# Kernel optimization log

Hardware: AMD Instinct MI355X
Metric: run time of the kernel (lower is better)

Reference implementation:

```python
import jax, jax.numpy as jnp
import numpy as np

B, T, C, NH = 4, 827, 1024, 16
HS = C // NH
SCALE = 1.0 / float(np.sqrt(HS))


def setup_inputs() -> dict:
    key = jax.random.key(0)
    ks = jax.random.split(key, 16)
    d = {}
    d["x"] = jax.random.normal(ks[0], (B, T, C), jnp.float32)
    d["x_kv"] = jax.random.normal(ks[1], (B, T, C), jnp.float32)
    d["h"] = jax.random.normal(ks[2], (B, NH, T, T), jnp.float32) * 0.1
    for i, name in enumerate(["f01", "f02", "f12", "b01", "b02", "b12"]):
        d[name] = jax.random.uniform(ks[3 + i], (B, 256, 256), jnp.float32)
    for i, name in enumerate(["Wq", "Wk", "Wv", "Wp"]):
        d[name] = jax.random.normal(ks[9 + i], (C, C), jnp.float32) * 0.02
    for name in ["bq", "bk", "bv", "bp"]:
        d[name] = jnp.zeros((C,), jnp.float32)
    return d


def _sm(a):
    return jax.nn.softmax(a, axis=-1)


def reference(x, x_kv, h, f01, f02, f12, b01, b02, b12,
              Wq, bq, Wk, bk, Wv, bv, Wp, bp):
    Bb, Tt, Cc = x.shape

    def heads(t):  # [B,T,C] -> [B,NH,T,HS]
        return t.reshape(Bb, Tt, NH, HS).transpose(0, 2, 1, 3)

    q = heads(x @ Wq.T + bq)
    k = heads(x_kv @ Wk.T + bk)
    v = heads(x_kv @ Wv.T + bv)

    att = jnp.einsum('bhqd,bhkd->bhqk', q, k) * SCALE + h  # adaptive bias add

    # region-specific partial softmax (frame1->frame0, frame2->frame0, frame2->frame1)
    att = att.at[:, :, 285:541, 0:256].set(_sm(att[:, :, 285:541, 0:256]))
    att = att.at[:, :, 571:827, 0:256].set(_sm(att[:, :, 571:827, 0:256]))
    att = att.at[:, :, 571:827, 286:542].set(_sm(att[:, :, 571:827, 286:542]))

    # bidirectional epipolar maps (backward maps used transposed)
    b01t = b01.transpose(0, 2, 1)
    b02t = b02.transpose(0, 2, 1)
    b12t = b12.transpose(0, 2, 1)
    m12 = (f12 * b12t >= 0.1).astype(att.dtype)  # [B,256,256]

    # bi_epi_ratio (T==827 branch), computed BEFORE the multiplicative masking
    r3 = att[:, :, 571:827, 286:542]            # [B,NH,256,256]
    att_mean = r3.mean(-1)                       # [B,NH,256]
    att_mask_mean = (r3 * m12[:, None]).sum(-1) / m12.sum(-1)[:, None]
    bi_epi_ratio = att_mask_mean.mean(1) / att_mean.mean(1)  # [B,256]

    # att_for: forward-only masking (clone); att: forward*backward masking
    att_for = att
    att_for = att_for.at[:, :, 285:541, 0:256].multiply(f01[:, None])
    att_for = att_for.at[:, :, 571:827, 0:256].multiply(f02[:, None])
    att_for = att_for.at[:, :, 571:827, 286:542].multiply(f12[:, None])
    att = att.at[:, :, 285:541, 0:256].multiply((b01t * f01)[:, None])
    att = att.at[:, :, 571:827, 0:256].multiply((b02t * f02)[:, None])
    att = att.at[:, :, 571:827, 286:542].multiply((b12t * f12)[:, None])

    causal = jnp.tril(jnp.ones((Tt, Tt), dtype=bool))
    aw = jnp.where(causal, att, -jnp.inf)
    # re-softmax of the already masked+multiplied regions (overwrites, then global softmax)
    aw = aw.at[:, :, 571:827, 0:256].set(_sm(att[:, :, 571:827, 0:256]))
    aw = aw.at[:, :, 571:827, 286:542].set(_sm(att[:, :, 571:827, 286:542]))
    aw = _sm(aw)

    y = jnp.einsum('bhqk,bhkd->bhqd', aw, v)
    y = y.transpose(0, 2, 1, 3).reshape(Bb, Tt, Cc)
    y = y @ Wp.T + bp  # resid dropout is identity (pdrop=0 / eval)
    return y, bi_epi_ratio
```

## Files before the change

### kernel.cpp

```cpp
#include <hip/hip_runtime.h>
#include <cstdint>
#include <cstddef>

#define Tn  827
#define Cn  1024
#define BTn 3308
#define TPn 832
#define YSZ 3387392

typedef unsigned short u16;
typedef unsigned short u16x4 __attribute__((ext_vector_type(4)));
typedef __bf16 bf16_t;
typedef bf16_t bf16x8 __attribute__((ext_vector_type(8)));
typedef float f32x4 __attribute__((ext_vector_type(4)));

#define GLD(gp, lp) __builtin_amdgcn_global_load_lds( \
    (__attribute__((address_space(1))) void*)(gp),    \
    (__attribute__((address_space(3))) void*)(lp), 16, 0, 0)

__device__ inline u16 f32_to_bf16(float f) {
  union { float f; unsigned u; } v; v.f = f;
  unsigned u = v.u;
  u += 0x7fffu + ((u >> 16) & 1u);
  return (u16)(u >> 16);
}

__global__ __launch_bounds__(256)
void cvt_all_k(const float* __restrict__ x, const float* __restrict__ xkv,
               const float* __restrict__ wq, const float* __restrict__ wk,
               const float* __restrict__ wv, const float* __restrict__ wp,
               u16* __restrict__ xb, u16* __restrict__ xkb,
               u16* __restrict__ wqb, u16* __restrict__ wkb,
               u16* __restrict__ wvb, u16* __restrict__ wpb,
               u16* __restrict__ Vt)
{
  const long NX = 846848;
  const long NW = 262144;
  long qidx = (long)blockIdx.x * 256 + threadIdx.x;
  const float* s; u16* d; long base;
  float sc = 1.0f;
  if (qidx < NX)            { s = x;   d = xb;  base = qidx; }
  else if (qidx < 2 * NX)   { s = xkv; d = xkb; base = qidx - NX; }
  else {
    long w = qidx - 2 * NX;
    int wi = (int)(w / NW);
    if (wi >= 4) {
      long p = w - 4 * NW;
      if (p < 20480) {
        int row = (int)(p / 5);
        int col = 827 + (int)(p - (long)row * 5);
        Vt[(size_t)row * TPn + col] = 0;
      }
      return;
    }
    base = w - (long)wi * NW;
    if      (wi == 0) { s = wq; d = wqb; sc = 0.125f; }
    else if (wi == 1) { s = wk; d = wkb; }
    else if (wi == 2) { s = wv; d = wvb; }
    else              { s = wp; d = wpb; }
  }
  const float4 v = *(const float4*)(s + base * 4);
  u16x4 o;
  o.x = f32_to_bf16(v.x * sc); o.y = f32_to_bf16(v.y * sc);
  o.z = f32_to_bf16(v.z * sc); o.w = f32_to_bf16(v.w * sc);
  *(u16x4*)(d + base * 4) = o;
}

__global__ __launch_bounds__(256)
void gemm_qkv_k(const u16* __restrict__ xb, const u16* __restrict__ xkb,
                const u16* __restrict__ wqb, const u16* __restrict__ wkb,
                const u16* __restrict__ wvb,
                const float* __restrict__ bq, const float* __restrict__ bk,
                const float* __restrict__ bv,
                u16* __restrict__ Qb, u16* __restrict__ Kb, u16* __restrict__ Vt)
{
  const int zz = blockIdx.z;
  const u16* A  = (zz == 0) ? xb : xkb;
  const u16* Bw = (zz == 0) ? wqb : (zz == 1) ? wkb : wvb;
  const float* bias = (zz == 0) ? bq : (zz == 1) ? bk : bv;
  const float bsc = (zz == 0) ? 0.125f : 1.0f;

  const int tid  = threadIdx.x;
  const int lane = tid & 63;
  const int wave = tid >> 6;
  const int wm = wave >> 1, wn = wave & 1;
  const int m0 = blockIdx.x * 128;
  const int n0 = blockIdx.y * 128;

  __shared__ u16 As[128 * 32];
  __shared__ u16 Bs[128 * 32];

  f32x4 acc[4][4];
  const f32x4 zero4 = {0.f, 0.f, 0.f, 0.f};
  #pragma unroll
  for (int i = 0; i < 4; ++i)
    #pragma unroll
    for (int j = 0; j < 4; ++j)
      acc[i][j] = zero4;

  for (int kt = 0; kt < 32; ++kt) {
    const int k0 = kt << 5;
    __syncthreads();
    #pragma unroll
    for (int it = 0; it < 2; ++it) {
      const int cbase = it * 256 + wave * 64;
      const int c  = cbase + lane;
      const int r  = c >> 2;
      const int ko = (c & 3) << 3;
      if (m0 + r < BTn)
        GLD(A  + (size_t)(m0 + r) * Cn + k0 + ko, As + cbase * 8);
      GLD(Bw + (size_t)(n0 + r) * Cn + k0 + ko, Bs + cbase * 8);
    }
    __syncthreads();

    bf16x8 af[4], bfr[4];
    #pragma unroll
    for (int i = 0; i < 4; ++i) {
      const int r = wm * 64 + i * 16 + (lane & 15);
      af[i] = *(const bf16x8*)(As + r * 32 + ((lane >> 4) << 3));
    }
    #pragma unroll
    for (int j = 0; j < 4; ++j) {
      const int r = wn * 64 + j * 16 + (lane & 15);
      bfr[j] = *(const bf16x8*)(Bs + r * 32 + ((lane >> 4) << 3));
    }
    #pragma unroll
    for (int i = 0; i < 4; ++i)
      #pragma unroll
      for (int j = 0; j < 4; ++j)
        acc[i][j] = __builtin_amdgcn_mfma_f32_16x16x32_bf16(af[i], bfr[j], acc[i][j], 0, 0, 0);
  }

  const int cq = lane >> 4, cl = lane & 15;
  if (zz < 2) {
    u16* D = (zz == 0) ? Qb : Kb;
    #pragma unroll
    for (int i = 0; i < 4; ++i) {
      #pragma unroll
      for (int j = 0; j < 4; ++j) {
        const int rb  = m0 + wm * 64 + i * 16 + cq * 4;
        const int col = n0 + wn * 64 + j * 16 + cl;
        const float bc = bias[col] * bsc;
        #pragma unroll
        for (int r = 0; r < 4; ++r) {
          const int row = rb + r;
          if (row < BTn) D[(size_t)row * Cn + col] = f32_to_bf16(acc[i][j][r] + bc);
        }
      }
    }
  } else {
    #pragma unroll
    for (int j = 0; j < 4; ++j) {
      const int col = n0 + wn * 64 + j * 16 + cl;
      const int hh = col >> 6, dd = col & 63;
      const float bc = bias[col];
      #pragma unroll
      for (int i = 0; i < 4; ++i) {
        const int rb = m0 + wm * 64 + i * 16 + cq * 4;
        #pragma unroll
        for (int r = 0; r < 4; ++r) {
          const int row = rb + r;
          if (row < BTn) {
            const int bb = row / Tn;
            const int t  = row - bb * Tn;
            Vt[((size_t)((bb * 16 + hh) * 64 + dd)) * TPn + t] = f32_to_bf16(acc[i][j][r] + bc);
          }
        }
      }
    }
  }
}

template<int BM, int BN, int MODE>
__global__ __launch_bounds__(256)
void gemm_k(const u16* __restrict__ Aall, const u16* __restrict__ Ball,
            const float* __restrict__ bias, float* __restrict__ Cf,
            u16* __restrict__ Cb, int M, int N, int K, int lda, int ldb, int ldc)
{
  static_assert(BM == 128, "BM fixed at 128");
  constexpr int TM = BM / 32;
  constexpr int TN = BN / 32;

  const int tid  = threadIdx.x;
  const int lane = tid & 63;
  const int wave = tid >> 6;
  const int wm = wave >> 1, wn = wave & 1;
  const int m0 = blockIdx.x * BM;
  const int n0 = blockIdx.y * BN;

  __shared__ u16 As[BM * 32];
  __shared__ u16 Bs[BN * 32];

  f32x4 acc[TM][TN];
  const f32x4 zero4 = {0.f, 0.f, 0.f, 0.f};
  #pragma unroll
  for (int i = 0; i < TM; ++i)
    #pragma unroll
    for (int j = 0; j < TN; ++j)
      acc[i][j] = zero4;

  const int nk = K >> 5;

  for (int kt = 0; kt < nk; ++kt) {
    const int k0 = kt << 5;
    __syncthreads();
    #pragma unroll
    for (int it = 0; it < BM / 64; ++it) {
      const int cbase = it * 256 + wave * 64;
      const int c  = cbase + lane;
      const int r  = c >> 2;
      const int ko = (c & 3) << 3;
      if (m0 + r < M)
        GLD(Aall + (size_t)(m0 + r) * lda + k0 + ko, As + cbase * 8);
    }
    #pragma unroll
    for (int it = 0; it < BN / 64; ++it) {
      const int cbase = it * 256 + wave * 64;
      const int c  = cbase + lane;
      const int r  = c >> 2;
      const int ko = (c & 3) << 3;
      if (n0 + r < N)
        GLD(Ball + (size_t)(n0 + r) * ldb + k0 + ko, Bs + cbase * 8);
    }
    __syncthreads();

    bf16x8 af[TM], bfr[TN];
    #pragma unroll
    for (int i = 0; i < TM; ++i) {
      const int r = wm * 64 + i * 16 + (lane & 15);
      af[i] = *(const bf16x8*)(As + r * 32 + ((lane >> 4) << 3));
    }
    #pragma unroll
    for (int j = 0; j < TN; ++j) {
      const int r = wn * (TN * 16) + j * 16 + (lane & 15);
      bfr[j] = *(const bf16x8*)(Bs + r * 32 + ((lane >> 4) << 3));
    }
    #pragma unroll
    for (int i = 0; i < TM; ++i)
      #pragma unroll
      for (int j = 0; j < TN; ++j)
        acc[i][j] = __builtin_amdgcn_mfma_f32_16x16x32_bf16(af[i], bfr[j], acc[i][j], 0, 0, 0);
  }

  const int cq = lane >> 4, cl = lane & 15;
  #pragma unroll
  for (int i = 0; i < TM; ++i) {
    #pragma unroll
    for (int j = 0; j < TN; ++j) {
      const int rb  = m0 + wm * 64 + i * 16 + cq * 4;
      const int col = n0 + wn * (TN * 16) + j * 16 + cl;
      #pragma unroll
      for (int r = 0; r < 4; ++r) {
        const int row = rb + r;
        const float v = acc[i][j][r];
        if constexpr (MODE == 0) {
          if (row < M) Cb[(size_t)row * ldc + col] = f32_to_bf16(v + bias[col]);
        } else {
          if (row < M) Cf[(size_t)row * ldc + col] = v + bias[col];
        }
      }
    }
  }
}

__global__ __launch_bounds__(256)
void btrans_k(const float* __restrict__ b01, const float* __restrict__ b02,
              const float* __restrict__ b12, float* __restrict__ bT)
{
  const int mb = blockIdx.z;
  const int rg = mb >> 2, bb = mb & 3;
  const float* src = (rg == 0 ? b01 : rg == 1 ? b02 : b12) + (size_t)bb * 65536;
  float* dst = bT + (size_t)mb * 65536;
  const int i0 = blockIdx.x * 64, j0 = blockIdx.y * 64;
  __shared__ float tile[64 * 65];
  const int tid = threadIdx.x;
  #pragma unroll
  for (int rep = 0; rep < 16; ++rep) {
    const int idx = rep * 256 + tid;
    const int jj = idx >> 6, ii = idx & 63;
    tile[ii * 65 + jj] = src[(size_t)(j0 + jj) * 256 + i0 + ii];
  }
  __syncthreads();
  #pragma unroll
  for (int rep = 0; rep < 16; ++rep) {
    const int idx = rep * 256 + tid;
    const int ii = idx >> 6, jj = idx & 63;
    dst[(size_t)(i0 + ii) * 256 + j0 + jj] = tile[ii * 65 + jj];
  }
}

__global__ __launch_bounds__(256)
void regfused_k(const u16* __restrict__ Qb, const u16* __restrict__ Kb,
                const float* __restrict__ hsrc,
                const float* __restrict__ f01, const float* __restrict__ f02,
                const float* __restrict__ f12, const float* __restrict__ bT,
                float* __restrict__ Sreg, float* __restrict__ mmOut,
                float* __restrict__ amOut)
{
  const int zr = blockIdx.y;
  const int rg = zr % 3;
  const int z  = zr / 3;
  const int b = z >> 4, hh = z & 15;
  const int qoff = (rg == 0) ? 285 : 571;
  const int koff = (rg == 2) ? 286 : 0;
  const int m0 = blockIdx.x * 64;

  const int tid = threadIdx.x, lane = tid & 63, wave = tid >> 6;
  const int quad = lane >> 4, cl = lane & 15;

  __shared__ u16 Qs[2 * 2048];
  __shared__ u16 Ks[2 * 8192];

  const u16* qsrc = Qb + ((size_t)(b * Tn + qoff + m0)) * Cn + hh * 64;
  const u16* ksrc = Kb + ((size_t)(b * Tn + koff)) * Cn + hh * 64;
  {
    const int r  = tid >> 2;
    const int ko = (tid & 3) << 3;
    #pragma unroll
    for (int p = 0; p < 2; ++p) {
      GLD(qsrc + (size_t)r * Cn + p * 32 + ko, &Qs[p * 2048 + wave * 512]);
      #pragma unroll
      for (int it = 0; it < 4; ++it) {
        const int c  = it * 256 + tid;
        const int rr = c >> 2;
        const int kko = (c & 3) << 3;
        GLD(ksrc + (size_t)rr * Cn + p * 32 + kko,
            &Ks[p * 8192 + it * 2048 + wave * 512]);
      }
    }
  }
  __syncthreads();

  bf16x8 qa[2];
  #pragma unroll
  for (int p = 0; p < 2; ++p)
    qa[p] = *(const bf16x8*)(&Qs[p * 2048 + (wave * 16 + cl) * 32 + quad * 8]);

  f32x4 acc[16];
  const f32x4 zero4 = {0.f, 0.f, 0.f, 0.f};
  #pragma unroll
  for (int n = 0; n < 16; ++n) acc[n] = zero4;

  #pragma unroll
  for (int p = 0; p < 2; ++p)
    #pragma unroll
    for (int n = 0; n < 16; ++n) {
      const bf16x8 kb = *(const bf16x8*)(&Ks[p * 8192 + (n * 16 + cl) * 32 + quad * 8]);
      acc[n] = __builtin_amdgcn_mfma_f32_16x16x32_bf16(qa[p], kb, acc[n], 0, 0, 0);
    }

  const int i0 = m0 + wave * 16 + quad * 4;
  const float* hp = hsrc + (size_t)z * Tn * Tn + (size_t)(qoff + i0) * Tn + koff + cl;
  #pragma unroll
  for (int nb = 0; nb < 4; ++nb) {
    float hv[4][4];
    #pragma unroll
    for (int n2 = 0; n2 < 4; ++n2)
      #pragma unroll
      for (int r = 0; r < 4; ++r)
        hv[n2][r] = hp[(size_t)r * Tn + (nb * 4 + n2) * 16];
    #pragma unroll
    for (int n2 = 0; n2 < 4; ++n2)
      #pragma unroll
      for (int r = 0; r < 4; ++r)
        acc[nb * 4 + n2][r] = acc[nb * 4 + n2][r] + hv[n2][r];
  }

  float red[4];
  #pragma unroll
  for (int r = 0; r < 4; ++r) {
    float m = acc[0][r];
    #pragma unroll
    for (int n = 1; n < 16; ++n) m = fmaxf(m, acc[n][r]);
    m = fmaxf(m, __shfl_xor(m, 1));
    m = fmaxf(m, __shfl_xor(m, 2));
    m = fmaxf(m, __shfl_xor(m, 4));
    m = fmaxf(m, __shfl_xor(m, 8));
    red[r] = m;
  }
  #pragma unroll
  for (int n = 0; n < 16; ++n)
    #pragma unroll
    for (int r = 0; r < 4; ++r)
      acc[n][r] = __expf(acc[n][r] - red[r]);
  #pragma unroll
  for (int r = 0; r < 4; ++r) {
    float s = 0.f;
    #pragma unroll
    for (int n = 0; n < 16; ++n) s += acc[n][r];
    s += __shfl_xor(s, 1); s += __shfl_xor(s, 2);
    s += __shfl_xor(s, 4); s += __shfl_xor(s, 8);
    const float inv = 1.f / s;
    #pragma unroll
    for (int n = 0; n < 16; ++n) acc[n][r] *= inv;
  }

  const float* fp  = (rg == 0) ? f01 : (rg == 1) ? f02 : f12;
  const float* fpb = fp + ((size_t)b * 256 + i0) * 256 + cl;
  const float* bpb = bT + (((size_t)(rg * 4 + b)) << 16) + (size_t)i0 * 256 + cl;
  float msum[4] = {0.f, 0.f, 0.f, 0.f};
  float mcnt[4] = {0.f, 0.f, 0.f, 0.f};
  float asum[4] = {0.f, 0.f, 0.f, 0.f};
  #pragma unroll
  for (int nb = 0; nb < 4; ++nb) {
    float fv[4][4], bv[4][4];
    #pragma unroll
    for (int n2 = 0; n2 < 4; ++n2)
      #pragma unroll
      for (int r = 0; r < 4; ++r) {
        fv[n2][r] = fpb[(size_t)r * 256 + (nb * 4 + n2) * 16];
        bv[n2][r] = bpb[(size_t)r * 256 + (nb * 4 + n2) * 16];
      }
    #pragma unroll
    for (int n2 = 0; n2 < 4; ++n2)
      #pragma unroll
      for (int r = 0; r < 4; ++r) {
        const int n = nb * 4 + n2;
        const float prod = fv[n2][r] * bv[n2][r];
        if (rg == 2) {
          const float mk = (prod >= 0.1f) ? 1.f : 0.f;
          msum[r] += acc[n][r] * mk;
          mcnt[r] += mk;
          asum[r] += acc[n][r];
        }
        acc[n][r] *= prod;
      }
  }
  if (rg == 2) {
    #pragma unroll
    for (int r = 0; r < 4; ++r) {
      msum[r] += __shfl_xor(msum[r], 1); msum[r] += __shfl_xor(msum[r], 2);
      msum[r] += __shfl_xor(msum[r], 4); msum[r] += __shfl_xor(msum[r], 8);
      mcnt[r] += __shfl_xor(mcnt[r], 1); mcnt[r] += __shfl_xor(mcnt[r], 2);
      mcnt[r] += __shfl_xor(mcnt[r], 4); mcnt[r] += __shfl_xor(mcnt[r], 8);
      asum[r] += __shfl_xor(asum[r], 1); asum[r] += __shfl_xor(asum[r], 2);
      asum[r] += __shfl_xor(asum[r], 4); asum[r] += __shfl_xor(asum[r], 8);
    }
    if (cl == 0) {
      #pragma unroll
      for (int r = 0; r < 4; ++r) {
        const int idx = ((b * 16 + hh) << 8) + i0 + r;
        mmOut[idx] = msum[r] / mcnt[r];
        amOut[idx] = asum[r] * (1.f / 256.f);
      }
    }
  }

  if (rg != 0) {
    #pragma unroll
    for (int r = 0; r < 4; ++r) {
      float m = acc[0][r];
      #pragma unroll
      for (int n = 1; n < 16; ++n) m = fmaxf(m, acc[n][r]);
      m = fmaxf(m, __shfl_xor(m, 1));
      m = fmaxf(m, __shfl_xor(m, 2));
      m = fmaxf(m, __shfl_xor(m, 4));
      m = fmaxf(m, __shfl_xor(m, 8));
      red[r] = m;
    }
    #pragma unroll
    for (int n = 0; n < 16; ++n)
      #pragma unroll
      for (int r = 0; r < 4; ++r)
        acc[n][r] = __expf(acc[n][r] - red[r]);
    #pragma unroll
    for (int r = 0; r < 4; ++r) {
      float s = 0.f;
      #pragma unroll
      for (int n = 0; n < 16; ++n) s += acc[n][r];
      s += __shfl_xor(s, 1); s += __shfl_xor(s, 2);
      s += __shfl_xor(s, 4); s += __shfl_xor(s, 8);
      const float inv = 1.f / s;
      #pragma unroll
      for (int n = 0; n < 16; ++n) acc[n][r] *= inv;
    }
  }
  float* outp = Sreg + (((size_t)zr) << 16) + (size_t)i0 * 256 + cl;
  #pragma unroll
  for (int n = 0; n < 16; ++n)
    #pragma unroll
    for (int r = 0; r < 4; ++r)
      outp[(size_t)r * 256 + n * 16] = acc[n][r];
}

__global__ __launch_bounds__(256)
void flash_k(const u16* __restrict__ Qb, const u16* __restrict__ Kb,
             const u16* __restrict__ Vt, const float* __restrict__ hsrc,
             const float* __restrict__ Sreg, u16* __restrict__ ya)
{
  const int bid = blockIdx.x;
  const int zlow = bid & 7;
  const int t = bid >> 3;
  const int qt = 12 - (t % 13);
  const int zhigh = t / 13;
  const int z = zhigh * 8 + zlow;
  const int b = z >> 4, hh = z & 15;
  const int q0 = qt * 64;

  const int tid = threadIdx.x;
  const int lane = tid & 63;
  const int wave = tid >> 6;
  const int quad = lane >> 4;
  const int cl = lane & 15;

  __shared__ u16 Ps[4][2][512];

  const u16* qbase = Qb + ((size_t)(b * Tn + q0 + wave * 16 + cl)) * Cn
                        + hh * 64 + quad * 8;
  bf16x8 qa[2];
  qa[0] = *(const bf16x8*)(qbase);
  qa[1] = *(const bf16x8*)(qbase + 32);

  const u16* kbase = Kb + ((size_t)(b * Tn + cl)) * Cn + hh * 64 + quad * 8;
  const u16* vbase = Vt + ((size_t)(z * 64 + cl)) * TPn + quad * 8;

  const int qrow_base = q0 + wave * 16 + quad * 4;
  const size_t hbase = (size_t)z * Tn * Tn;
  const float* hrow[4];
  const float* preg1[4];
  const float* preg2[4];
  int cat[4];
  #pragma unroll
  for (int r = 0; r < 4; ++r) {
    const int qq = qrow_base + r;
    const int qc = (qq < Tn) ? qq : (Tn - 1);
    hrow[r] = hsrc + hbase + (size_t)qc * Tn;
    if (qq >= 571 && qq < Tn) {
      cat[r] = 2;
      preg1[r] = Sreg + (((size_t)(z * 3 + 1)) << 16) + (size_t)(qq - 571) * 256;
      preg2[r] = Sreg + (((size_t)(z * 3 + 2)) << 16) + (size_t)(qq - 571) * 256 - 286;
    } else if (qq >= 285 && qq < 541) {
      cat[r] = 1;
      preg1[r] = Sreg + (((size_t)(z * 3 + 0)) << 16) + (size_t)(qq - 285) * 256;
      preg2[r] = hrow[r];
    } else {
      cat[r] = 0;
      preg1[r] = hrow[r];
      preg2[r] = hrow[r];
    }
  }

#define GATHER(hv_, rm_, k0_) do {                                        \
    rm_ = 0;                                                              \
    if ((k0_) < 542) {                                                    \
      _Pragma("unroll")                                                   \
      for (int j = 0; j < 4; ++j) {                                       \
        const int kk = (k0_) + j * 16 + cl;                               \
        _Pragma("unroll")                                                 \
        for (int r = 0; r < 4; ++r) {                                     \
          const float* p = hrow[r] + kk;                                  \
          bool isr = false;                                               \
          if (cat[r] == 2) {                                              \
            if (kk < 256)       { p = preg1[r] + kk; isr = true; }        \
            else if (kk >= 286 && kk < 542) { p = preg2[r] + kk; isr = true; } \
          } else if (cat[r] == 1) {                                       \
            if (kk < 256)       { p = preg1[r] + kk; isr = true; }        \
          }                                                               \
          hv_[j * 4 + r] = *p;                                            \
          if (isr) rm_ |= 1u << (j * 4 + r);                              \
        }                                                                 \
      }                                                                   \
    } else {                                                              \
      _Pragma("unroll")                                                   \
      for (int j = 0; j < 4; ++j) {                                       \
        const int kk = (k0_) + j * 16 + cl;                               \
        _Pragma("unroll")                                                 \
        for (int r = 0; r < 4; ++r) hv_[j * 4 + r] = hrow[r][kk];         \
      }                                                                   \
    }                                                                     \
  } while (0)

  f32x4 Oa[4];
  const f32x4 zero4 = {0.f, 0.f, 0.f, 0.f};
  Oa[0] = zero4; Oa[1] = zero4; Oa[2] = zero4; Oa[3] = zero4;
  float mrow[4] = {-3.0e38f, -3.0e38f, -3.0e38f, -3.0e38f};
  float lrow[4] = {0.f, 0.f, 0.f, 0.f};

  for (int kt = 0; kt <= qt; ++kt) {
    const int k0 = kt * 64;
    const bool diag = (kt == qt);

    bf16x8 kf[2][4];
    #pragma unroll
    for (int p = 0; p < 2; ++p)
      #pragma unroll
      for (int n = 0; n < 4; ++n)
        kf[p][n] = *(const bf16x8*)(kbase + (size_t)(k0 + n * 16) * Cn + p * 32);
    float hv[16]; unsigned rmask;
    GATHER(hv, rmask, k0);

    f32x4 sa[4];
    sa[0] = zero4; sa[1] = zero4; sa[2] = zero4; sa[3] = zero4;
    __builtin_amdgcn_s_setprio(1);
    #pragma unroll
    for (int p = 0; p < 2; ++p)
      #pragma unroll
      for (int n = 0; n < 4; ++n)
        sa[n] = __builtin_amdgcn_mfma_f32_16x16x32_bf16(qa[p], kf[p][n], sa[n], 0, 0, 0);
    __builtin_amdgcn_s_setprio(0);

    #pragma unroll
    for (int r = 0; r < 4; ++r) {
      const int qq = qrow_base + r;
      float sv[4];
      #pragma unroll
      for (int j = 0; j < 4; ++j) {
        const int kk = k0 + j * 16 + cl;
        const float vv = ((rmask >> (j * 4 + r)) & 1)
                             ? hv[j * 4 + r]
                             : sa[j][r] + hv[j * 4 + r];
        sv[j] = (diag && !(kk <= qq && qq < Tn)) ? -3.0e38f : vv;
      }
      float mx = fmaxf(fmaxf(sv[0], sv[1]), fmaxf(sv[2], sv[3]));
      mx = fmaxf(mx, __shfl_xor(mx, 1));
      mx = fmaxf(mx, __shfl_xor(mx, 2));
      mx = fmaxf(mx, __shfl_xor(mx, 4));
      mx = fmaxf(mx, __shfl_xor(mx, 8));
      const float mnew = fmaxf(mrow[r], mx);
      const float alpha = __expf(mrow[r] - mnew);
      mrow[r] = mnew;
      float ps[4], psum = 0.f;
      #pragma unroll
      for (int j = 0; j < 4; ++j) { ps[j] = __expf(sv[j] - mnew); psum += ps[j]; }
      psum += __shfl_xor(psum, 1);
      psum += __shfl_xor(psum, 2);
      psum += __shfl_xor(psum, 4);
      psum += __shfl_xor(psum, 8);
      lrow[r] = lrow[r] * alpha + psum;
      #pragma unroll
      for (int n = 0; n < 4; ++n) Oa[n][r] *= alpha;
      #pragma unroll
      for (int j = 0; j < 4; ++j)
        Ps[wave][j >> 1][(quad * 4 + r) * 32 + (j & 1) * 16 + cl] = f32_to_bf16(ps[j]);
    }

    bf16x8 vf[2][4];
    #pragma unroll
    for (int p = 0; p < 2; ++p)
      #pragma unroll
      for (int n = 0; n < 4; ++n)
        vf[p][n] = *(const bf16x8*)(vbase + (size_t)(n * 16) * TPn + k0 + p * 32);

    __builtin_amdgcn_s_setprio(1);
    #pragma unroll
    for (int p = 0; p < 2; ++p) {
      const bf16x8 pa = *(const bf16x8*)(&Ps[wave][p][cl * 32 + quad * 8]);
      #pragma unroll
      for (int n = 0; n < 4; ++n)
        Oa[n] = __builtin_amdgcn_mfma_f32_16x16x32_bf16(pa, vf[p][n], Oa[n], 0, 0, 0);
    }
    __builtin_amdgcn_s_setprio(0);
  }
#undef GATHER

  #pragma unroll
  for (int r = 0; r < 4; ++r) {
    const int qq = qrow_base + r;
    if (qq >= Tn) continue;
    const float inv = 1.f / lrow[r];
    u16* op = ya + ((size_t)(b * Tn + qq)) * Cn + hh * 64;
    #pragma unroll
    for (int n = 0; n < 4; ++n)
      op[n * 16 + cl] = f32_to_bf16(Oa[n][r] * inv);
  }
}

__global__ __launch_bounds__(256)
void ratio_k(const float* __restrict__ mm, const float* __restrict__ am,
             float* __restrict__ out)
{
  const int idx = blockIdx.x * 256 + threadIdx.x;
  const int b = idx >> 8, i = idx & 255;
  float smm = 0.f, sam = 0.f;
  #pragma unroll
  for (int hh = 0; hh < 16; ++hh) {
    smm += mm[(b * 16 + hh) * 256 + i];
    sam += am[(b * 16 + hh) * 256 + i];
  }
  out[idx] = smm / sam;
}

extern "C" void kernel_launch(void* const* d_in, const int* in_sizes, int n_in,
                              void* d_out, int out_size, void* d_ws, size_t ws_size,
                              hipStream_t stream)
{
  (void)in_sizes; (void)n_in; (void)out_size;

  const float* x   = (const float*)d_in[0];
  const float* xkv = (const float*)d_in[1];
  const float* hb  = (const float*)d_in[2];
  const float* f01 = (const float*)d_in[3];
  const float* f02 = (const float*)d_in[4];
  const float* f12 = (const float*)d_in[5];
  const float* b01 = (const float*)d_in[6];
  const float* b02 = (const float*)d_in[7];
  const float* b12 = (const float*)d_in[8];
  const float* Wq  = (const float*)d_in[9];
  const float* Wk  = (const float*)d_in[10];
  const float* Wv  = (const float*)d_in[11];
  const float* Wp  = (const float*)d_in[12];
  const float* bq  = (const float*)d_in[13];
  const float* bk  = (const float*)d_in[14];
  const float* bv  = (const float*)d_in[15];
  const float* bp  = (const float*)d_in[16];
  float* out = (float*)d_out;

  char* ws = (char*)d_ws;
  u16* xb   = (u16*)(ws + 0);
  u16* xkb  = (u16*)(ws + 6774784);
  u16* wqb  = (u16*)(ws + 13549568);
  u16* wkb  = (u16*)(ws + 15646720);
  u16* wvb  = (u16*)(ws + 17743872);
  u16* wpb  = (u16*)(ws + 19841024);
  u16* Qb   = (u16*)(ws + 21938176);
  u16* Kb   = (u16*)(ws + 28712960);
  u16* Vt   = (u16*)(ws + 42262528);
  u16* ya   = (u16*)(ws + 49078272);
  float* Sreg = (float*)(ws + 55853056);
  float* bT = (float*)(ws + 106184704);
  float* mm = (float*)(ws + 109330432);
  float* am = (float*)(ws + 109395968);
  const size_t need = 109461504;
  if (ws_size < need) return;

  cvt_all_k<<<dim3(10792), 256, 0, stream>>>(x, xkv, Wq, Wk, Wv, Wp,
                                             xb, xkb, wqb, wkb, wvb, wpb, Vt);
  btrans_k<<<dim3(4, 4, 12), 256, 0, stream>>>(b01, b02, b12, bT);
  gemm_qkv_k<<<dim3(26, 8, 3), 256, 0, stream>>>(xb, xkb, wqb, wkb, wvb,
                                                 bq, bk, bv, Qb, Kb, Vt);
  regfused_k<<<dim3(4, 192), 256, 0, stream>>>(Qb, Kb, hb, f01, f02, f12, bT,
                                               Sreg, mm, am);
  ratio_k<<<dim3(4), 256, 0, stream>>>(mm, am, out + YSZ);
  flash_k<<<dim3(832), 256, 0, stream>>>(Qb, Kb, Vt, hb, Sreg, ya);
  gemm_k<128, 64, 3><<<dim3(26, 16, 1), 256, 0, stream>>>(ya, wpb, bp, out, nullptr,
                                                          BTn, Cn, Cn, Cn, Cn, Cn);
}
```

Measured before the change: 470.0 us.

## Split flash attention into single-wave blocks with balanced causal row pairs

The flash kernel goes from 4-wave blocks over 64-row query tiles to 1-wave blocks. Each block handles two 16-row query strips paired from opposite ends (s and 51-s) so causal work per block is roughly even, and the V loads are hoisted ahead of the QK MFMAs. The QKV GEMM tile width is halved from 128 to 64 columns, doubling the grid to raise occupancy and parallelism. In exchange, K/V tiles are no longer shared across four waves in a block, so global and L2 traffic for K and V rises, and the narrower GEMM tile lowers data reuse.

```diff
diff --git a/kernel.cpp b/kernel.cpp
--- a/kernel.cpp
+++ b/kernel.cpp
@@ -85,17 +85,17 @@
   const int wave = tid >> 6;
   const int wm = wave >> 1, wn = wave & 1;
   const int m0 = blockIdx.x * 128;
-  const int n0 = blockIdx.y * 128;
+  const int n0 = blockIdx.y * 64;
 
   __shared__ u16 As[128 * 32];
-  __shared__ u16 Bs[128 * 32];
-
-  f32x4 acc[4][4];
+  __shared__ u16 Bs[64 * 32];
+
+  f32x4 acc[4][2];
   const f32x4 zero4 = {0.f, 0.f, 0.f, 0.f};
   #pragma unroll
   for (int i = 0; i < 4; ++i)
     #pragma unroll
-    for (int j = 0; j < 4; ++j)
+    for (int j = 0; j < 2; ++j)
       acc[i][j] = zero4;
 
   for (int kt = 0; kt < 32; ++kt) {
@@ -108,26 +108,30 @@
       const int r  = c >> 2;
       const int ko = (c & 3) << 3;
       if (m0 + r < BTn)
-        GLD(A  + (size_t)(m0 + r) * Cn + k0 + ko, As + cbase * 8);
-      GLD(Bw + (size_t)(n0 + r) * Cn + k0 + ko, Bs + cbase * 8);
+        GLD(A + (size_t)(m0 + r) * Cn + k0 + ko, As + cbase * 8);
+    }
+    {
+      const int r  = tid >> 2;
+      const int ko = (tid & 3) << 3;
+      GLD(Bw + (size_t)(n0 + r) * Cn + k0 + ko, Bs + (tid >> 2) * 32 + ko);
     }
     __syncthreads();
 
-    bf16x8 af[4], bfr[4];
+    bf16x8 af[4], bfr[2];
     #pragma unroll
     for (int i = 0; i < 4; ++i) {
       const int r = wm * 64 + i * 16 + (lane & 15);
       af[i] = *(const bf16x8*)(As + r * 32 + ((lane >> 4) << 3));
     }
     #pragma unroll
-    for (int j = 0; j < 4; ++j) {
-      const int r = wn * 64 + j * 16 + (lane & 15);
+    for (int j = 0; j < 2; ++j) {
+      const int r = wn * 32 + j * 16 + (lane & 15);
       bfr[j] = *(const bf16x8*)(Bs + r * 32 + ((lane >> 4) << 3));
     }
     #pragma unroll
     for (int i = 0; i < 4; ++i)
       #pragma unroll
-      for (int j = 0; j < 4; ++j)
+      for (int j = 0; j < 2; ++j)
         acc[i][j] = __builtin_amdgcn_mfma_f32_16x16x32_bf16(af[i], bfr[j], acc[i][j], 0, 0, 0);
   }
 
@@ -137,9 +141,9 @@
     #pragma unroll
     for (int i = 0; i < 4; ++i) {
       #pragma unroll
-      for (int j = 0; j < 4; ++j) {
+      for (int j = 0; j < 2; ++j) {
         const int rb  = m0 + wm * 64 + i * 16 + cq * 4;
-        const int col = n0 + wn * 64 + j * 16 + cl;
+        const int col = n0 + wn * 32 + j * 16 + cl;
         const float bc = bias[col] * bsc;
         #pragma unroll
         for (int r = 0; r < 4; ++r) {
@@ -150,8 +154,8 @@
     }
   } else {
     #pragma unroll
-    for (int j = 0; j < 4; ++j) {
-      const int col = n0 + wn * 64 + j * 16 + cl;
+    for (int j = 0; j < 2; ++j) {
+      const int col = n0 + wn * 32 + j * 16 + cl;
       const int hh = col >> 6, dd = col & 63;
       const float bc = bias[col];
       #pragma unroll
@@ -483,185 +487,180 @@
       outp[(size_t)r * 256 + n * 16] = acc[n][r];
 }
 
-__global__ __launch_bounds__(256)
+__global__ __launch_bounds__(64, 2)
 void flash_k(const u16* __restrict__ Qb, const u16* __restrict__ Kb,
              const u16* __restrict__ Vt, const float* __restrict__ hsrc,
              const float* __restrict__ Sreg, u16* __restrict__ ya)
 {
-  const int bid = blockIdx.x;
-  const int zlow = bid & 7;
-  const int t = bid >> 3;
-  const int qt = 12 - (t % 13);
-  const int zhigh = t / 13;
-  const int z = zhigh * 8 + zlow;
+  const int bid  = blockIdx.x;
+  const int z    = bid & 63;
+  const int pair = bid >> 6;
   const int b = z >> 4, hh = z & 15;
-  const int q0 = qt * 64;
-
-  const int tid = threadIdx.x;
-  const int lane = tid & 63;
-  const int wave = tid >> 6;
+
+  const int lane = threadIdx.x & 63;
   const int quad = lane >> 4;
   const int cl = lane & 15;
 
-  __shared__ u16 Ps[4][2][512];
-
-  const u16* qbase = Qb + ((size_t)(b * Tn + q0 + wave * 16 + cl)) * Cn
-                        + hh * 64 + quad * 8;
-  bf16x8 qa[2];
-  qa[0] = *(const bf16x8*)(qbase);
-  qa[1] = *(const bf16x8*)(qbase + 32);
+  __shared__ u16 Ps[2][512];
 
   const u16* kbase = Kb + ((size_t)(b * Tn + cl)) * Cn + hh * 64 + quad * 8;
   const u16* vbase = Vt + ((size_t)(z * 64 + cl)) * TPn + quad * 8;
-
-  const int qrow_base = q0 + wave * 16 + quad * 4;
   const size_t hbase = (size_t)z * Tn * Tn;
-  const float* hrow[4];
-  const float* preg1[4];
-  const float* preg2[4];
-  int cat[4];
-  #pragma unroll
-  for (int r = 0; r < 4; ++r) {
-    const int qq = qrow_base + r;
-    const int qc = (qq < Tn) ? qq : (Tn - 1);
-    hrow[r] = hsrc + hbase + (size_t)qc * Tn;
-    if (qq >= 571 && qq < Tn) {
-      cat[r] = 2;
-      preg1[r] = Sreg + (((size_t)(z * 3 + 1)) << 16) + (size_t)(qq - 571) * 256;
-      preg2[r] = Sreg + (((size_t)(z * 3 + 2)) << 16) + (size_t)(qq - 571) * 256 - 286;
-    } else if (qq >= 285 && qq < 541) {
-      cat[r] = 1;
-      preg1[r] = Sreg + (((size_t)(z * 3 + 0)) << 16) + (size_t)(qq - 285) * 256;
-      preg2[r] = hrow[r];
-    } else {
-      cat[r] = 0;
-      preg1[r] = hrow[r];
-      preg2[r] = hrow[r];
-    }
-  }
-
-#define GATHER(hv_, rm_, k0_) do {                                        \
-    rm_ = 0;                                                              \
-    if ((k0_) < 542) {                                                    \
-      _Pragma("unroll")                                                   \
-      for (int j = 0; j < 4; ++j) {                                       \
-        const int kk = (k0_) + j * 16 + cl;                               \
-        _Pragma("unroll")                                                 \
-        for (int r = 0; r < 4; ++r) {                                     \
-          const float* p = hrow[r] + kk;                                  \
-          bool isr = false;                                               \
-          if (cat[r] == 2) {                                              \
-            if (kk < 256)       { p = preg1[r] + kk; isr = true; }        \
-            else if (kk >= 286 && kk < 542) { p = preg2[r] + kk; isr = true; } \
-          } else if (cat[r] == 1) {                                       \
-            if (kk < 256)       { p = preg1[r] + kk; isr = true; }        \
-          }                                                               \
-          hv_[j * 4 + r] = *p;                                            \
-          if (isr) rm_ |= 1u << (j * 4 + r);                              \
-        }                                                                 \
-      }                                                                   \
-    } else {                                                              \
-      _Pragma("unroll")                                                   \
-      for (int j = 0; j < 4; ++j) {                                       \
-        const int kk = (k0_) + j * 16 + cl;                               \
-        _Pragma("unroll")                                                 \
-        for (int r = 0; r < 4; ++r) hv_[j * 4 + r] = hrow[r][kk];         \
-      }                                                                   \
-    }                                                                     \
-  } while (0)
-
-  f32x4 Oa[4];
   const f32x4 zero4 = {0.f, 0.f, 0.f, 0.f};
-  Oa[0] = zero4; Oa[1] = zero4; Oa[2] = zero4; Oa[3] = zero4;
-  float mrow[4] = {-3.0e38f, -3.0e38f, -3.0e38f, -3.0e38f};
-  float lrow[4] = {0.f, 0.f, 0.f, 0.f};
-
-  for (int kt = 0; kt <= qt; ++kt) {
-    const int k0 = kt * 64;
-    const bool diag = (kt == qt);
-
-    bf16x8 kf[2][4];
-    #pragma unroll
-    for (int p = 0; p < 2; ++p)
-      #pragma unroll
-      for (int n = 0; n < 4; ++n)
-        kf[p][n] = *(const bf16x8*)(kbase + (size_t)(k0 + n * 16) * Cn + p * 32);
-    float hv[16]; unsigned rmask;
-    GATHER(hv, rmask, k0);
-
-    f32x4 sa[4];
-    sa[0] = zero4; sa[1] = zero4; sa[2] = zero4; sa[3] = zero4;
-    __builtin_amdgcn_s_setprio(1);
-    #pragma unroll
-    for (int p = 0; p < 2; ++p)
-      #pragma unroll
-      for (int n = 0; n < 4; ++n)
-        sa[n] = __builtin_amdgcn_mfma_f32_16x16x32_bf16(qa[p], kf[p][n], sa[n], 0, 0, 0);
-    __builtin_amdgcn_s_setprio(0);
-
+
+  #pragma unroll 1
+  for (int ss = 0; ss < 2; ++ss) {
+    const int s  = ss ? (51 - pair) : pair;
+    const int nk = (s >> 2) + 1;
+    const int q0 = s * 16;
+
+    const u16* qbase = Qb + ((size_t)(b * Tn + q0 + cl)) * Cn + hh * 64 + quad * 8;
+    bf16x8 qa[2];
+    qa[0] = *(const bf16x8*)(qbase);
+    qa[1] = *(const bf16x8*)(qbase + 32);
+
+    const int qrow_base = q0 + quad * 4;
+    const float* hrow[4];
+    const float* preg1[4];
+    const float* preg2[4];
+    int cat[4];
     #pragma unroll
     for (int r = 0; r < 4; ++r) {
       const int qq = qrow_base + r;
-      float sv[4];
-      #pragma unroll
-      for (int j = 0; j < 4; ++j) {
-        const int kk = k0 + j * 16 + cl;
-        const float vv = ((rmask >> (j * 4 + r)) & 1)
-                             ? hv[j * 4 + r]
-                             : sa[j][r] + hv[j * 4 + r];
-        sv[j] = (diag && !(kk <= qq && qq < Tn)) ? -3.0e38f : vv;
-      }
-      float mx = fmaxf(fmaxf(sv[0], sv[1]), fmaxf(sv[2], sv[3]));
-      mx = fmaxf(mx, __shfl_xor(mx, 1));
-      mx = fmaxf(mx, __shfl_xor(mx, 2));
-      mx = fmaxf(mx, __shfl_xor(mx, 4));
-      mx = fmaxf(mx, __shfl_xor(mx, 8));
-      const float mnew = fmaxf(mrow[r], mx);
-      const float alpha = __expf(mrow[r] - mnew);
-      mrow[r] = mnew;
-      float ps[4], psum = 0.f;
-      #pragma unroll
-      for (int j = 0; j < 4; ++j) { ps[j] = __expf(sv[j] - mnew); psum += ps[j]; }
-      psum += __shfl_xor(psum, 1);
-      psum += __shfl_xor(psum, 2);
-      psum += __shfl_xor(psum, 4);
-      psum += __shfl_xor(psum, 8);
-      lrow[r] = lrow[r] * alpha + psum;
-      #pragma unroll
-      for (int n = 0; n < 4; ++n) Oa[n][r] *= alpha;
-      #pragma unroll
-      for (int j = 0; j < 4; ++j)
-        Ps[wave][j >> 1][(quad * 4 + r) * 32 + (j & 1) * 16 + cl] = f32_to_bf16(ps[j]);
-    }
-
-    bf16x8 vf[2][4];
-    #pragma unroll
-    for (int p = 0; p < 2; ++p)
+      const int qc = (qq < Tn) ? qq : (Tn - 1);
+      hrow[r] = hsrc + hbase + (size_t)qc * Tn;
+      if (qq >= 571 && qq < Tn) {
+        cat[r] = 2;
+        preg1[r] = Sreg + (((size_t)(z * 3 + 1)) << 16) + (size_t)(qq - 571) * 256;
+        preg2[r] = Sreg + (((size_t)(z * 3 + 2)) << 16) + (size_t)(qq - 571) * 256 - 286;
+      } else if (qq >= 285 && qq < 541) {
+        cat[r] = 1;
+        preg1[r] = Sreg + (((size_t)(z * 3 + 0)) << 16) + (size_t)(qq - 285) * 256;
+        preg2[r] = hrow[r];
+      } else {
+        cat[r] = 0;
+        preg1[r] = hrow[r];
+        preg2[r] = hrow[r];
+      }
+    }
+
+    f32x4 Oa[4];
+    Oa[0] = zero4; Oa[1] = zero4; Oa[2] = zero4; Oa[3] = zero4;
+    float mrow[4] = {-3.0e38f, -3.0e38f, -3.0e38f, -3.0e38f};
+    float lrow[4] = {0.f, 0.f, 0.f, 0.f};
+
+    for (int kt = 0; kt < nk; ++kt) {
+      const int k0 = kt * 64;
+      const bool diag = (kt == nk - 1);
+
+      bf16x8 kf[2][4];
+      #pragma unroll
+      for (int p = 0; p < 2; ++p)
+        #pragma unroll
+        for (int n = 0; n < 4; ++n)
+          kf[p][n] = *(const bf16x8*)(kbase + (size_t)(k0 + n * 16) * Cn + p * 32);
+
+      float hv[16]; unsigned rmask = 0;
+      if (k0 < 542) {
+        #pragma unroll
+        for (int j = 0; j < 4; ++j) {
+          const int kk = k0 + j * 16 + cl;
+          #pragma unroll
+          for (int r = 0; r < 4; ++r) {
+            const float* p = hrow[r] + kk;
+            bool isr = false;
+            if (cat[r] == 2) {
+              if (kk < 256)                   { p = preg1[r] + kk; isr = true; }
+              else if (kk >= 286 && kk < 542) { p = preg2[r] + kk; isr = true; }
+            } else if (cat[r] == 1) {
+              if (kk < 256)                   { p = preg1[r] + kk; isr = true; }
+            }
+            hv[j * 4 + r] = *p;
+            if (isr) rmask |= 1u << (j * 4 + r);
+          }
+        }
+      } else {
+        #pragma unroll
+        for (int j = 0; j < 4; ++j) {
+          const int kk = k0 + j * 16 + cl;
+          #pragma unroll
+          for (int r = 0; r < 4; ++r) hv[j * 4 + r] = hrow[r][kk];
+        }
+      }
+
+      bf16x8 vf[2][4];
+      #pragma unroll
+      for (int p = 0; p < 2; ++p)
+        #pragma unroll
+        for (int n = 0; n < 4; ++n)
+          vf[p][n] = *(const bf16x8*)(vbase + (size_t)(n * 16) * TPn + k0 + p * 32);
+
+      f32x4 sa[4];
+      sa[0] = zero4; sa[1] = zero4; sa[2] = zero4; sa[3] = zero4;
+      __builtin_amdgcn_s_setprio(1);
+      #pragma unroll
+      for (int p = 0; p < 2; ++p)
+        #pragma unroll
+        for (int n = 0; n < 4; ++n)
+          sa[n] = __builtin_amdgcn_mfma_f32_16x16x32_bf16(qa[p], kf[p][n], sa[n], 0, 0, 0);
+      __builtin_amdgcn_s_setprio(0);
+
+      #pragma unroll
+      for (int r = 0; r < 4; ++r) {
+        const int qq = qrow_base + r;
+        float sv[4];
+        #pragma unroll
+        for (int j = 0; j < 4; ++j) {
+          const int kk = k0 + j * 16 + cl;
+          const float vv = ((rmask >> (j * 4 + r)) & 1)
+                               ? hv[j * 4 + r]
+                               : sa[j][r] + hv[j * 4 + r];
+          sv[j] = (diag && !(kk <= qq && qq < Tn)) ? -3.0e38f : vv;
+        }
+        float mx = fmaxf(fmaxf(sv[0], sv[1]), fmaxf(sv[2], sv[3]));
+        mx = fmaxf(mx, __shfl_xor(mx, 1));
+        mx = fmaxf(mx, __shfl_xor(mx, 2));
+        mx = fmaxf(mx, __shfl_xor(mx, 4));
+        mx = fmaxf(mx, __shfl_xor(mx, 8));
+        const float mnew = fmaxf(mrow[r], mx);
+        const float alpha = __expf(mrow[r] - mnew);
+        mrow[r] = mnew;
+        float ps[4], psum = 0.f;
+        #pragma unroll
+        for (int j = 0; j < 4; ++j) { ps[j] = __expf(sv[j] - mnew); psum += ps[j]; }
+        psum += __shfl_xor(psum, 1);
+        psum += __shfl_xor(psum, 2);
+        psum += __shfl_xor(psum, 4);
+        psum += __shfl_xor(psum, 8);
+        lrow[r] = lrow[r] * alpha + psum;
+        #pragma unroll
+        for (int n = 0; n < 4; ++n) Oa[n][r] *= alpha;
+        #pragma unroll
+        for (int j = 0; j < 4; ++j)
+          Ps[j >> 1][(quad * 4 + r) * 32 + (j & 1) * 16 + cl] = f32_to_bf16(ps[j]);
+      }
+
+      __builtin_amdgcn_s_setprio(1);
+      #pragma unroll
+      for (int p = 0; p < 2; ++p) {
+        const bf16x8 pa = *(const bf16x8*)(&Ps[p][cl * 32 + quad * 8]);
+        #pragma unroll
+        for (int n = 0; n < 4; ++n)
+          Oa[n] = __builtin_amdgcn_mfma_f32_16x16x32_bf16(pa, vf[p][n], Oa[n], 0, 0, 0);
+      }
+      __builtin_amdgcn_s_setprio(0);
+    }
+
+    #pragma unroll
+    for (int r = 0; r < 4; ++r) {
+      const int qq = qrow_base + r;
+      if (qq >= Tn) continue;
+      const float inv = 1.f / lrow[r];
+      u16* op = ya + ((size_t)(b * Tn + qq)) * Cn + hh * 64;
       #pragma unroll
       for (int n = 0; n < 4; ++n)
-        vf[p][n] = *(const bf16x8*)(vbase + (size_t)(n * 16) * TPn + k0 + p * 32);
-
-    __builtin_amdgcn_s_setprio(1);
-    #pragma unroll
-    for (int p = 0; p < 2; ++p) {
-      const bf16x8 pa = *(const bf16x8*)(&Ps[wave][p][cl * 32 + quad * 8]);
-      #pragma unroll
-      for (int n = 0; n < 4; ++n)
-        Oa[n] = __builtin_amdgcn_mfma_f32_16x16x32_bf16(pa, vf[p][n], Oa[n], 0, 0, 0);
-    }
-    __builtin_amdgcn_s_setprio(0);
-  }
-#undef GATHER
-
-  #pragma unroll
-  for (int r = 0; r < 4; ++r) {
-    const int qq = qrow_base + r;
-    if (qq >= Tn) continue;
-    const float inv = 1.f / lrow[r];
-    u16* op = ya + ((size_t)(b * Tn + qq)) * Cn + hh * 64;
-    #pragma unroll
-    for (int n = 0; n < 4; ++n)
-      op[n * 16 + cl] = f32_to_bf16(Oa[n][r] * inv);
+        op[n * 16 + cl] = f32_to_bf16(Oa[n][r] * inv);
+    }
   }
 }
 
@@ -726,12 +725,12 @@
   cvt_all_k<<<dim3(10792), 256, 0, stream>>>(x, xkv, Wq, Wk, Wv, Wp,
                                              xb, xkb, wqb, wkb, wvb, wpb, Vt);
   btrans_k<<<dim3(4, 4, 12), 256, 0, stream>>>(b01, b02, b12, bT);
-  gemm_qkv_k<<<dim3(26, 8, 3), 256, 0, stream>>>(xb, xkb, wqb, wkb, wvb,
-                                                 bq, bk, bv, Qb, Kb, Vt);
+  gemm_qkv_k<<<dim3(26, 16, 3), 256, 0, stream>>>(xb, xkb, wqb, wkb, wvb,
+                                                  bq, bk, bv, Qb, Kb, Vt);
   regfused_k<<<dim3(4, 192), 256, 0, stream>>>(Qb, Kb, hb, f01, f02, f12, bT,
                                                Sreg, mm, am);
   ratio_k<<<dim3(4), 256, 0, stream>>>(mm, am, out + YSZ);
-  flash_k<<<dim3(832), 256, 0, stream>>>(Qb, Kb, Vt, hb, Sreg, ya);
+  flash_k<<<dim3(1664), 64, 0, stream>>>(Qb, Kb, Vt, hb, Sreg, ya);
   gemm_k<128, 64, 3><<<dim3(26, 16, 1), 256, 0, stream>>>(ya, wpb, bp, out, nullptr,
                                                           BTn, Cn, Cn, Cn, Cn, Cn);
 }
```

New measurement: 440.4 us. 1.07x faster.
